# Kernel optimization log

Hardware: AMD Instinct MI355X
Metric: run time of the kernel (lower is better)

Reference implementation:

```python
import jax, jax.numpy as jnp
import numpy as np

HIDDEN = 1024

def setup_inputs() -> dict:
    key = jax.random.key(0)
    k1, k2, k3, k4, k5 = jax.random.split(key, 5)
    B, T, E2, H = 32, 2048, 1024, HIDDEN
    scale = 1.0 / np.sqrt(H)
    x = jax.random.normal(k1, (B, T, E2), dtype=jnp.float32)
    W_ih = jax.random.uniform(k2, (4 * H, E2), minval=-scale, maxval=scale, dtype=jnp.float32)
    W_hh = jax.random.uniform(k3, (4 * H, H), minval=-scale, maxval=scale, dtype=jnp.float32)
    b_ih = jax.random.uniform(k4, (4 * H,), minval=-scale, maxval=scale, dtype=jnp.float32)
    b_hh = jax.random.uniform(k5, (4 * H,), minval=-scale, maxval=scale, dtype=jnp.float32)
    return {"x": x, "W_ih": W_ih, "W_hh": W_hh, "b_ih": b_ih, "b_hh": b_hh}

def reference(x, W_ih, W_hh, b_ih, b_hh):
    B, T, _ = x.shape
    H = W_hh.shape[1]
    # Precompute input contribution for all timesteps: [T, B, 4H]
    x_proj = jnp.einsum('bte,ge->tbg', x, W_ih) + b_ih + b_hh

    def step(carry, xp_t):
        h, c = carry
        gates = xp_t + h @ W_hh.T  # [B, 4H]
        i, f, g, o = jnp.split(gates, 4, axis=-1)  # torch gate order i,f,g,o
        i = jax.nn.sigmoid(i)
        f = jax.nn.sigmoid(f)
        g = jnp.tanh(g)
        o = jax.nn.sigmoid(o)
        c_new = f * c + i * g
        h_new = o * jnp.tanh(c_new)
        return (h_new, c_new), None

    h0 = jnp.zeros((B, H), dtype=x.dtype)
    c0 = jnp.zeros((B, H), dtype=x.dtype)
    (h_t, c_t), _ = jax.lax.scan(step, (h0, c0), x_proj)
    return (h_t, c_t)
```

## Files before the change

### kernel.cpp

```cpp
#include <hip/hip_runtime.h>
#include <stdint.h>

#define T_STEPS 2048
#define HID 1024
#define G4 4096
#define NWG 64

typedef __attribute__((ext_vector_type(8))) short short8;
typedef __attribute__((ext_vector_type(4))) float float4v;
typedef __attribute__((ext_vector_type(4))) unsigned int uint4v;
typedef unsigned long long ull;

#define HBUF_OFF 0ull
#define FLAG_OFF 131072ull
#define DT_OFF   132608ull
#define CST_OFF  135168ull
#define XP_OFF   0x100000ull

__device__ inline unsigned short f2bf(float f) {
  union { float f; unsigned int u; } v; v.f = f;
  unsigned int u = v.u;
  return (unsigned short)((u + 0x7fffu + ((u >> 16) & 1u)) >> 16);
}
__device__ inline float bf2f(unsigned short h) {
  union { unsigned int u; float f; } v; v.u = ((unsigned int)h) << 16;
  return v.f;
}
__device__ inline short8 pack8(float4 a, float4 b) {
  short8 r;
  r[0] = (short)f2bf(a.x); r[1] = (short)f2bf(a.y);
  r[2] = (short)f2bf(a.z); r[3] = (short)f2bf(a.w);
  r[4] = (short)f2bf(b.x); r[5] = (short)f2bf(b.y);
  r[6] = (short)f2bf(b.z); r[7] = (short)f2bf(b.w);
  return r;
}

__global__ void dtype_sniff(const unsigned short* __restrict__ w,
                            unsigned int* __restrict__ dt) {
  __shared__ int red[256];
  const int tid = threadIdx.x;
  int cnt = 0;
#pragma unroll
  for (int i = 0; i < 4; i++) {
    unsigned short h = w[tid * 4 + i];
    unsigned e = (h >> 7) & 0xFF;
    if (h == 0 || (e >= 100 && e <= 123)) cnt++;
  }
  red[tid] = cnt;
  __syncthreads();
  for (int s = 128; s > 0; s >>= 1) {
    if (tid < s) red[tid] += red[tid + s];
    __syncthreads();
  }
  if (tid == 0) dt[0] = (red[0] >= 922) ? 1u : 0u;
}

__global__ __launch_bounds__(256) void xproj_gemm(
    const void* __restrict__ x, const void* __restrict__ Wih,
    const void* __restrict__ bih, const void* __restrict__ bhh,
    unsigned short* __restrict__ xp, int t0,
    const unsigned int* __restrict__ dt)
{
  __shared__ char smem[32768];
  __shared__ float bias_s[128];
  unsigned short* As = (unsigned short*)smem;
  unsigned short* Bs = (unsigned short*)(smem + 10240);

  const bool isbf = (*dt != 0);

  const int bid = blockIdx.x;
  const int panel = bid >> 9;
  const int within = bid & 511;
  const int nt = within & 31;
  const int mt = (panel << 4) + (within >> 5);
  const int m0 = mt * 128;
  const int n0 = nt * 128;
  const int tl0 = m0 >> 5;

  const int tid = threadIdx.x;
  if (tid < 128) {
    bias_s[tid] = isbf
        ? bf2f(((const unsigned short*)bih)[n0 + tid]) +
          bf2f(((const unsigned short*)bhh)[n0 + tid])
        : ((const float*)bih)[n0 + tid] + ((const float*)bhh)[n0 + tid];
  }

  const int w = tid >> 6, lane = tid & 63;
  const int quad = lane >> 4, lr = lane & 15;
  const int wm = (w & 1) * 64, wn = (w >> 1) * 64;

  float4v acc[4][4];
#pragma unroll
  for (int i = 0; i < 4; i++)
#pragma unroll
    for (int j = 0; j < 4; j++) acc[i][j] = (float4v){0.f, 0.f, 0.f, 0.f};

  const int r = tid >> 1, half = tid & 1;
  const size_t aoff =
      ((size_t)(r & 31) * T_STEPS + (size_t)(t0 + tl0 + (r >> 5))) * HID + half * 16;
  const size_t boff = (size_t)(n0 + r) * HID + half * 16;
  unsigned short* adst = As + r * 40 + half * 16;
  unsigned short* bdst = Bs + r * 40 + half * 16;

  for (int k0 = 0; k0 < HID; k0 += 32) {
    __syncthreads();
    if (isbf) {
      const unsigned short* a16 = (const unsigned short*)x + aoff + k0;
      const unsigned short* b16 = (const unsigned short*)Wih + boff + k0;
      *(short8*)(adst)     = *(const short8*)(a16);
      *(short8*)(adst + 8) = *(const short8*)(a16 + 8);
      *(short8*)(bdst)     = *(const short8*)(b16);
      *(short8*)(bdst + 8) = *(const short8*)(b16 + 8);
    } else {
      const float4* af = (const float4*)((const float*)x + aoff + k0);
      const float4* bf = (const float4*)((const float*)Wih + boff + k0);
      float4 a0 = af[0], a1 = af[1], a2 = af[2], a3 = af[3];
      float4 b0 = bf[0], b1 = bf[1], b2 = bf[2], b3 = bf[3];
      *(short8*)(adst)     = pack8(a0, a1);
      *(short8*)(adst + 8) = pack8(a2, a3);
      *(short8*)(bdst)     = pack8(b0, b1);
      *(short8*)(bdst + 8) = pack8(b2, b3);
    }
    __syncthreads();
    short8 afr[4], bfr[4];
#pragma unroll
    for (int i = 0; i < 4; i++)
      afr[i] = *(const short8*)(As + (wm + i * 16 + lr) * 40 + quad * 8);
#pragma unroll
    for (int j = 0; j < 4; j++)
      bfr[j] = *(const short8*)(Bs + (wn + j * 16 + lr) * 40 + quad * 8);
#pragma unroll
    for (int i = 0; i < 4; i++)
#pragma unroll
      for (int j = 0; j < 4; j++)
        acc[i][j] = __builtin_amdgcn_mfma_f32_16x16x32_bf16(afr[i], bfr[j], acc[i][j], 0, 0, 0);
  }

  __syncthreads();
  unsigned short* ep = (unsigned short*)smem;
#pragma unroll
  for (int i = 0; i < 4; i++)
#pragma unroll
    for (int j = 0; j < 4; j++)
#pragma unroll
      for (int rr = 0; rr < 4; rr++) {
        int ml = wm + i * 16 + quad * 4 + rr;
        int nl = wn + j * 16 + lr;
        float v = acc[i][j][rr] + bias_s[nl];
        ep[(((ml >> 5) * 128) + nl) * 32 + (ml & 31)] = f2bf(v);
      }
  __syncthreads();
#pragma unroll
  for (int tl = 0; tl < 4; tl++) {
    const uint4* s4 = (const uint4*)(smem + tl * 8192);
    uint4* d4 = (uint4*)(xp + ((size_t)(tl0 + tl) * G4 + n0) * 32);
    for (int i = tid; i < 512; i += 256) d4[i] = s4[i];
  }
}

__global__ __launch_bounds__(256, 1) void lstm_rec(
    const void* __restrict__ Whh,
    const unsigned short* __restrict__ xp,
    unsigned short* __restrict__ hbuf,
    unsigned int* __restrict__ flags,
    float* __restrict__ cstate,
    void* __restrict__ out,
    int t0, int tc,
    const unsigned int* __restrict__ dt)
{
  __shared__ __align__(16) unsigned short hs[32768];
  __shared__ float gbuf[64][33];

  const bool isbf = (*dt != 0);
  const int wg = blockIdx.x;
  const int tid = threadIdx.x;
  const int w = tid >> 6, lane = tid & 63;
  const int quad = lane >> 4, lr = lane & 15;

  short8 bfrag[32];
  {
    const size_t grow = (size_t)w * HID + wg * 16 + lr;
    if (isbf) {
      const unsigned short* wrow = (const unsigned short*)Whh + grow * HID;
#pragma unroll
      for (int s = 0; s < 32; s++)
        bfrag[s] = *(const short8*)(wrow + s * 32 + quad * 8);
    } else {
      const float* wrow = (const float*)Whh + grow * HID;
#pragma unroll
      for (int s = 0; s < 32; s++) {
        float4 f0 = *(const float4*)(wrow + s * 32 + quad * 8);
        float4 f1 = *(const float4*)(wrow + s * 32 + quad * 8 + 4);
        bfrag[s] = pack8(f0, f1);
      }
    }
  }

  const int gb = lane >> 1, gh = lane & 1;
  const int gc = 2 * w + gh;
  const int gslot = (gc & 3) ^ ((gb >> 1) & 3);
  char* gdst = (char*)hs + ((gc >> 2) * 2048 + gb * 64 + gslot * 16);

  const int qsw = quad ^ ((lr >> 1) & 3);
  const char* ga0 = (const char*)hs + lr * 64 + qsw * 16;
  const char* ga1 = (const char*)hs + (16 + lr) * 64 + qsw * 16;

  const int cb = 8 * w + (lane >> 3);
  const int ck = lane & 7;
  const int j0 = 2 * ck, j1 = j0 + 1;
  const int gc0 = wg * 16 + j0, gc1 = gc0 + 1;
  float cs0 = cstate[(size_t)cb * HID + gc0];
  float cs1 = cstate[(size_t)cb * HID + gc1];
  long budget = 50000000;

  for (int t = t0; t < t0 + tc; t++) {
    const unsigned short* xpt = xp + (size_t)(t - t0) * (G4 * 32);
    unsigned short rx0 = xpt[(size_t)gc0 * 32 + cb];
    unsigned short rx1 = xpt[(size_t)(HID + gc0) * 32 + cb];
    unsigned short rx2 = xpt[(size_t)(2 * HID + gc0) * 32 + cb];
    unsigned short rx3 = xpt[(size_t)(3 * HID + gc0) * 32 + cb];
    unsigned short rx4 = xpt[(size_t)gc1 * 32 + cb];
    unsigned short rx5 = xpt[(size_t)(HID + gc1) * 32 + cb];
    unsigned short rx6 = xpt[(size_t)(2 * HID + gc1) * 32 + cb];
    unsigned short rx7 = xpt[(size_t)(3 * HID + gc1) * 32 + cb];

    if (w == 0) {
      const unsigned target = (unsigned)t;
      const unsigned int* fp = flags + 4 * lane;
      for (;;) {
        uint4v f;
        asm volatile("global_load_dwordx4 %0, %1, off sc0 sc1\n\t"
                     "s_waitcnt vmcnt(0)"
                     : "=v"(f) : "v"(fp) : "memory");
        unsigned m01 = f[0] < f[1] ? f[0] : f[1];
        unsigned m23 = f[2] < f[3] ? f[2] : f[3];
        if ((m01 < m23 ? m01 : m23) >= target) break;
        if (--budget < 0) break;
        __builtin_amdgcn_s_sleep(1);
      }
    }
    __syncthreads();

    {
      const uint4v* src = (const uint4v*)(hbuf + (size_t)(t & 1) * 32768) + tid;
      uint4v v0, v1, v2, v3, v4, v5, v6, v7, v8, v9, v10, v11, v12, v13, v14, v15;
#define GL(i, dst) \
      asm volatile("global_load_dwordx4 %0, %1, off sc0 sc1" \
                   : "=v"(dst) : "v"(src + (i) * 256) : "memory")
      GL(0, v0);  GL(1, v1);  GL(2, v2);  GL(3, v3);
      GL(4, v4);  GL(5, v5);  GL(6, v6);  GL(7, v7);
      GL(8, v8);  GL(9, v9);  GL(10, v10); GL(11, v11);
      GL(12, v12); GL(13, v13); GL(14, v14); GL(15, v15);
#undef GL
      asm volatile("s_waitcnt vmcnt(0)" ::: "memory");
      *(uint4v*)(gdst + 0 * 4096)  = v0;  *(uint4v*)(gdst + 1 * 4096)  = v1;
      *(uint4v*)(gdst + 2 * 4096)  = v2;  *(uint4v*)(gdst + 3 * 4096)  = v3;
      *(uint4v*)(gdst + 4 * 4096)  = v4;  *(uint4v*)(gdst + 5 * 4096)  = v5;
      *(uint4v*)(gdst + 6 * 4096)  = v6;  *(uint4v*)(gdst + 7 * 4096)  = v7;
      *(uint4v*)(gdst + 8 * 4096)  = v8;  *(uint4v*)(gdst + 9 * 4096)  = v9;
      *(uint4v*)(gdst + 10 * 4096) = v10; *(uint4v*)(gdst + 11 * 4096) = v11;
      *(uint4v*)(gdst + 12 * 4096) = v12; *(uint4v*)(gdst + 13 * 4096) = v13;
      *(uint4v*)(gdst + 14 * 4096) = v14; *(uint4v*)(gdst + 15 * 4096) = v15;
    }
    __syncthreads();

    float4v acc00 = (float4v){0.f, 0.f, 0.f, 0.f};
    float4v acc01 = (float4v){0.f, 0.f, 0.f, 0.f};
    float4v acc10 = (float4v){0.f, 0.f, 0.f, 0.f};
    float4v acc11 = (float4v){0.f, 0.f, 0.f, 0.f};
#pragma unroll
    for (int s = 0; s < 32; s += 2) {
      short8 x00 = *(const short8*)(ga0 + (size_t)s * 2048);
      short8 x01 = *(const short8*)(ga0 + (size_t)s * 2048 + 2048);
      short8 x10 = *(const short8*)(ga1 + (size_t)s * 2048);
      short8 x11 = *(const short8*)(ga1 + (size_t)s * 2048 + 2048);
      acc00 = __builtin_amdgcn_mfma_f32_16x16x32_bf16(x00, bfrag[s],     acc00, 0, 0, 0);
      acc01 = __builtin_amdgcn_mfma_f32_16x16x32_bf16(x01, bfrag[s + 1], acc01, 0, 0, 0);
      acc10 = __builtin_amdgcn_mfma_f32_16x16x32_bf16(x10, bfrag[s],     acc10, 0, 0, 0);
      acc11 = __builtin_amdgcn_mfma_f32_16x16x32_bf16(x11, bfrag[s + 1], acc11, 0, 0, 0);
    }
    {
      float4v g0 = acc00 + acc01;
      float4v g1 = acc10 + acc11;
      const int lc = w * 16 + lr;
#pragma unroll
      for (int rr = 0; rr < 4; rr++) {
        gbuf[lc][quad * 4 + rr]      = g0[rr];
        gbuf[lc][16 + quad * 4 + rr] = g1[rr];
      }
    }
    __syncthreads();

    {
      float gi0 = gbuf[j0][cb]      + bf2f(rx0);
      float gf0 = gbuf[16 + j0][cb] + bf2f(rx1);
      float gg0 = gbuf[32 + j0][cb] + bf2f(rx2);
      float go0 = gbuf[48 + j0][cb] + bf2f(rx3);
      float si0 = 1.f / (1.f + __expf(-gi0));
      float sf0 = 1.f / (1.f + __expf(-gf0));
      float tg0 = tanhf(gg0);
      float so0 = 1.f / (1.f + __expf(-go0));
      cs0 = sf0 * cs0 + si0 * tg0;
      float hn0 = so0 * tanhf(cs0);

      float gi1 = gbuf[j1][cb]      + bf2f(rx4);
      float gf1 = gbuf[16 + j1][cb] + bf2f(rx5);
      float gg1 = gbuf[32 + j1][cb] + bf2f(rx6);
      float go1 = gbuf[48 + j1][cb] + bf2f(rx7);
      float si1 = 1.f / (1.f + __expf(-gi1));
      float sf1 = 1.f / (1.f + __expf(-gf1));
      float tg1 = tanhf(gg1);
      float so1 = 1.f / (1.f + __expf(-go1));
      cs1 = sf1 * cs1 + si1 * tg1;
      float hn1 = so1 * tanhf(cs1);

      unsigned pk = (unsigned)f2bf(hn0) | ((unsigned)f2bf(hn1) << 16);
      unsigned int* hb32 = (unsigned int*)hbuf;
      const unsigned idx = (unsigned)(((t + 1) & 1) * 16384 +
                                      wg * 256 + cb * 8 + ck);
      __hip_atomic_store(hb32 + idx, pk, __ATOMIC_RELAXED, __HIP_MEMORY_SCOPE_AGENT);

      if (t == T_STEPS - 1) {
        if (isbf) {
          unsigned short* ob = (unsigned short*)out;
          ob[(size_t)cb * HID + gc0] = f2bf(hn0);
          ob[(size_t)cb * HID + gc1] = f2bf(hn1);
          ob[32768 + (size_t)cb * HID + gc0] = f2bf(cs0);
          ob[32768 + (size_t)cb * HID + gc1] = f2bf(cs1);
        } else {
          float* of = (float*)out;
          of[(size_t)cb * HID + gc0] = hn0;
          of[(size_t)cb * HID + gc1] = hn1;
          of[32768 + (size_t)cb * HID + gc0] = cs0;
          of[32768 + (size_t)cb * HID + gc1] = cs1;
        }
      }
    }
    asm volatile("s_waitcnt vmcnt(0)" ::: "memory");
    if (lane == 0)
      __hip_atomic_store(&flags[wg * 4 + w], (unsigned)(t + 1), __ATOMIC_RELAXED,
                         __HIP_MEMORY_SCOPE_AGENT);
  }

  cstate[(size_t)cb * HID + gc0] = cs0;
  cstate[(size_t)cb * HID + gc1] = cs1;
}

extern "C" void kernel_launch(void* const* d_in, const int* in_sizes, int n_in,
                              void* d_out, int out_size, void* d_ws, size_t ws_size,
                              hipStream_t stream) {
  (void)in_sizes; (void)n_in; (void)out_size;
  const void* x   = d_in[0];
  const void* Wih = d_in[1];
  const void* Whh = d_in[2];
  const void* bih = d_in[3];
  const void* bhh = d_in[4];

  char* ws = (char*)d_ws;
  unsigned short* hbuf   = (unsigned short*)(ws + HBUF_OFF);
  unsigned int*   flags  = (unsigned int*)(ws + FLAG_OFF);
  unsigned int*   dt     = (unsigned int*)(ws + DT_OFF);
  float*          cstate = (float*)(ws + CST_OFF);
  unsigned short* xp     = (unsigned short*)(ws + XP_OFF);

  int tc = 2048;
  while (tc > 16 && XP_OFF + (size_t)tc * 262144ull > ws_size) tc >>= 1;

  hipMemsetAsync(ws, 0, CST_OFF + 131072, stream);

  hipLaunchKernelGGL(dtype_sniff, dim3(1), dim3(256), 0, stream,
                     (const unsigned short*)Wih, dt);

  for (int t0 = 0; t0 < T_STEPS; t0 += tc) {
    hipLaunchKernelGGL(xproj_gemm, dim3(tc * 8), dim3(256), 0, stream,
                       x, Wih, bih, bhh, xp, t0, dt);
    hipLaunchKernelGGL(lstm_rec, dim3(NWG), dim3(256), 0, stream,
                       Whh, xp, hbuf, flags, cstate, d_out, t0, tc, dt);
  }
}
```

Baseline: 12.78 ms.

## Split K across waves and load h directly into MFMA registers

Each wave now owns a quarter of the K dimension for all four gates instead of all K for one gate. Each wave loads its h slice straight from global memory into MFMA operand registers, which removes the shared-memory staging of h and one barrier. Partial sums from the four waves are reduced through a shared buffer. Every wave now polls its own subset of flags instead of only wave 0, which trades a block barrier for more polling traffic. The risk is that the per-wave global loads give less coalesced h fetches.

Result: faster. 11.12 ms (-13.0%).

```diff
diff --git a/kernel.cpp b/kernel.cpp
--- a/kernel.cpp
+++ b/kernel.cpp
@@ -168,8 +168,7 @@
     int t0, int tc,
     const unsigned int* __restrict__ dt)
 {
-  __shared__ __align__(16) unsigned short hs[32768];
-  __shared__ float gbuf[64][33];
+  __shared__ float gpart[4][64][36];
 
   const bool isbf = (*dt != 0);
   const int wg = blockIdx.x;
@@ -178,32 +177,24 @@
   const int quad = lane >> 4, lr = lane & 15;
 
   short8 bfrag[32];
-  {
-    const size_t grow = (size_t)w * HID + wg * 16 + lr;
+#pragma unroll
+  for (int q = 0; q < 4; q++) {
+    const size_t grow = (size_t)q * HID + wg * 16 + lr;
     if (isbf) {
       const unsigned short* wrow = (const unsigned short*)Whh + grow * HID;
 #pragma unroll
-      for (int s = 0; s < 32; s++)
-        bfrag[s] = *(const short8*)(wrow + s * 32 + quad * 8);
+      for (int s = 0; s < 8; s++)
+        bfrag[q * 8 + s] = *(const short8*)(wrow + w * 256 + s * 32 + quad * 8);
     } else {
       const float* wrow = (const float*)Whh + grow * HID;
 #pragma unroll
-      for (int s = 0; s < 32; s++) {
-        float4 f0 = *(const float4*)(wrow + s * 32 + quad * 8);
-        float4 f1 = *(const float4*)(wrow + s * 32 + quad * 8 + 4);
-        bfrag[s] = pack8(f0, f1);
-      }
-    }
-  }
-
-  const int gb = lane >> 1, gh = lane & 1;
-  const int gc = 2 * w + gh;
-  const int gslot = (gc & 3) ^ ((gb >> 1) & 3);
-  char* gdst = (char*)hs + ((gc >> 2) * 2048 + gb * 64 + gslot * 16);
-
-  const int qsw = quad ^ ((lr >> 1) & 3);
-  const char* ga0 = (const char*)hs + lr * 64 + qsw * 16;
-  const char* ga1 = (const char*)hs + (16 + lr) * 64 + qsw * 16;
+      for (int s = 0; s < 8; s++) {
+        float4 f0 = *(const float4*)(wrow + w * 256 + s * 32 + quad * 8);
+        float4 f1 = *(const float4*)(wrow + w * 256 + s * 32 + quad * 8 + 4);
+        bfrag[q * 8 + s] = pack8(f0, f1);
+      }
+    }
+  }
 
   const int cb = 8 * w + (lane >> 3);
   const int ck = lane & 7;
@@ -212,6 +203,8 @@
   float cs0 = cstate[(size_t)cb * HID + gc0];
   float cs1 = cstate[(size_t)cb * HID + gc1];
   long budget = 50000000;
+
+  const int gbase_off = w * 16384 + (quad >> 1) * 1024 + lr * 32 + (quad & 1) * 16;
 
   for (int t = t0; t < t0 + tc; t++) {
     const unsigned short* xpt = xp + (size_t)(t - t0) * (G4 * 32);
@@ -224,78 +217,66 @@
     unsigned short rx6 = xpt[(size_t)(2 * HID + gc1) * 32 + cb];
     unsigned short rx7 = xpt[(size_t)(3 * HID + gc1) * 32 + cb];
 
-    if (w == 0) {
+    {
       const unsigned target = (unsigned)t;
-      const unsigned int* fp = flags + 4 * lane;
-      for (;;) {
-        uint4v f;
-        asm volatile("global_load_dwordx4 %0, %1, off sc0 sc1\n\t"
-                     "s_waitcnt vmcnt(0)"
-                     : "=v"(f) : "v"(fp) : "memory");
-        unsigned m01 = f[0] < f[1] ? f[0] : f[1];
-        unsigned m23 = f[2] < f[3] ? f[2] : f[3];
-        if ((m01 < m23 ? m01 : m23) >= target) break;
+      const unsigned int* fp = flags + 64 * w + lane;
+      while (__hip_atomic_load(fp, __ATOMIC_RELAXED, __HIP_MEMORY_SCOPE_AGENT) < target) {
         if (--budget < 0) break;
         __builtin_amdgcn_s_sleep(1);
       }
     }
-    __syncthreads();
-
+
+    short8 av[2][8];
     {
-      const uint4v* src = (const uint4v*)(hbuf + (size_t)(t & 1) * 32768) + tid;
-      uint4v v0, v1, v2, v3, v4, v5, v6, v7, v8, v9, v10, v11, v12, v13, v14, v15;
-#define GL(i, dst) \
+      const char* gb = (const char*)hbuf + (size_t)(t & 1) * 65536 + gbase_off;
+#define GL(m, s) \
       asm volatile("global_load_dwordx4 %0, %1, off sc0 sc1" \
-                   : "=v"(dst) : "v"(src + (i) * 256) : "memory")
-      GL(0, v0);  GL(1, v1);  GL(2, v2);  GL(3, v3);
-      GL(4, v4);  GL(5, v5);  GL(6, v6);  GL(7, v7);
-      GL(8, v8);  GL(9, v9);  GL(10, v10); GL(11, v11);
-      GL(12, v12); GL(13, v13); GL(14, v14); GL(15, v15);
+                   : "=v"(av[m][s]) : "v"(gb + (s) * 2048 + (m) * 512) : "memory")
+      GL(0, 0); GL(1, 0); GL(0, 1); GL(1, 1);
+      GL(0, 2); GL(1, 2); GL(0, 3); GL(1, 3);
+      GL(0, 4); GL(1, 4); GL(0, 5); GL(1, 5);
+      GL(0, 6); GL(1, 6); GL(0, 7); GL(1, 7);
 #undef GL
       asm volatile("s_waitcnt vmcnt(0)" ::: "memory");
-      *(uint4v*)(gdst + 0 * 4096)  = v0;  *(uint4v*)(gdst + 1 * 4096)  = v1;
-      *(uint4v*)(gdst + 2 * 4096)  = v2;  *(uint4v*)(gdst + 3 * 4096)  = v3;
-      *(uint4v*)(gdst + 4 * 4096)  = v4;  *(uint4v*)(gdst + 5 * 4096)  = v5;
-      *(uint4v*)(gdst + 6 * 4096)  = v6;  *(uint4v*)(gdst + 7 * 4096)  = v7;
-      *(uint4v*)(gdst + 8 * 4096)  = v8;  *(uint4v*)(gdst + 9 * 4096)  = v9;
-      *(uint4v*)(gdst + 10 * 4096) = v10; *(uint4v*)(gdst + 11 * 4096) = v11;
-      *(uint4v*)(gdst + 12 * 4096) = v12; *(uint4v*)(gdst + 13 * 4096) = v13;
-      *(uint4v*)(gdst + 14 * 4096) = v14; *(uint4v*)(gdst + 15 * 4096) = v15;
-    }
-    __syncthreads();
-
-    float4v acc00 = (float4v){0.f, 0.f, 0.f, 0.f};
-    float4v acc01 = (float4v){0.f, 0.f, 0.f, 0.f};
-    float4v acc10 = (float4v){0.f, 0.f, 0.f, 0.f};
-    float4v acc11 = (float4v){0.f, 0.f, 0.f, 0.f};
-#pragma unroll
-    for (int s = 0; s < 32; s += 2) {
-      short8 x00 = *(const short8*)(ga0 + (size_t)s * 2048);
-      short8 x01 = *(const short8*)(ga0 + (size_t)s * 2048 + 2048);
-      short8 x10 = *(const short8*)(ga1 + (size_t)s * 2048);
-      short8 x11 = *(const short8*)(ga1 + (size_t)s * 2048 + 2048);
-      acc00 = __builtin_amdgcn_mfma_f32_16x16x32_bf16(x00, bfrag[s],     acc00, 0, 0, 0);
-      acc01 = __builtin_amdgcn_mfma_f32_16x16x32_bf16(x01, bfrag[s + 1], acc01, 0, 0, 0);
-      acc10 = __builtin_amdgcn_mfma_f32_16x16x32_bf16(x10, bfrag[s],     acc10, 0, 0, 0);
-      acc11 = __builtin_amdgcn_mfma_f32_16x16x32_bf16(x11, bfrag[s + 1], acc11, 0, 0, 0);
-    }
+      __builtin_amdgcn_sched_barrier(0);
+    }
+
+    float4v acc[2][4];
+#pragma unroll
+    for (int m = 0; m < 2; m++)
+#pragma unroll
+      for (int q = 0; q < 4; q++) acc[m][q] = (float4v){0.f, 0.f, 0.f, 0.f};
+#pragma unroll
+    for (int s = 0; s < 8; s++) {
+#pragma unroll
+      for (int q = 0; q < 4; q++) {
+        acc[0][q] = __builtin_amdgcn_mfma_f32_16x16x32_bf16(av[0][s], bfrag[q * 8 + s], acc[0][q], 0, 0, 0);
+        acc[1][q] = __builtin_amdgcn_mfma_f32_16x16x32_bf16(av[1][s], bfrag[q * 8 + s], acc[1][q], 0, 0, 0);
+      }
+    }
+
+    __syncthreads();
+#pragma unroll
+    for (int m = 0; m < 2; m++)
+#pragma unroll
+      for (int q = 0; q < 4; q++)
+        *(float4v*)&gpart[w][q * 16 + lr][m * 16 + quad * 4] = acc[m][q];
+    __syncthreads();
+
     {
-      float4v g0 = acc00 + acc01;
-      float4v g1 = acc10 + acc11;
-      const int lc = w * 16 + lr;
-#pragma unroll
-      for (int rr = 0; rr < 4; rr++) {
-        gbuf[lc][quad * 4 + rr]      = g0[rr];
-        gbuf[lc][16 + quad * 4 + rr] = g1[rr];
-      }
-    }
-    __syncthreads();
-
-    {
-      float gi0 = gbuf[j0][cb]      + bf2f(rx0);
-      float gf0 = gbuf[16 + j0][cb] + bf2f(rx1);
-      float gg0 = gbuf[32 + j0][cb] + bf2f(rx2);
-      float go0 = gbuf[48 + j0][cb] + bf2f(rx3);
+      float gi0 = bf2f(rx0), gf0 = bf2f(rx1), gg0 = bf2f(rx2), go0 = bf2f(rx3);
+      float gi1 = bf2f(rx4), gf1 = bf2f(rx5), gg1 = bf2f(rx6), go1 = bf2f(rx7);
+#pragma unroll
+      for (int p = 0; p < 4; p++) {
+        gi0 += gpart[p][j0][cb];
+        gf0 += gpart[p][16 + j0][cb];
+        gg0 += gpart[p][32 + j0][cb];
+        go0 += gpart[p][48 + j0][cb];
+        gi1 += gpart[p][j1][cb];
+        gf1 += gpart[p][16 + j1][cb];
+        gg1 += gpart[p][32 + j1][cb];
+        go1 += gpart[p][48 + j1][cb];
+      }
       float si0 = 1.f / (1.f + __expf(-gi0));
       float sf0 = 1.f / (1.f + __expf(-gf0));
       float tg0 = tanhf(gg0);
@@ -303,10 +284,6 @@
       cs0 = sf0 * cs0 + si0 * tg0;
       float hn0 = so0 * tanhf(cs0);
 
-      float gi1 = gbuf[j1][cb]      + bf2f(rx4);
-      float gf1 = gbuf[16 + j1][cb] + bf2f(rx5);
-      float gg1 = gbuf[32 + j1][cb] + bf2f(rx6);
-      float go1 = gbuf[48 + j1][cb] + bf2f(rx7);
       float si1 = 1.f / (1.f + __expf(-gi1));
       float sf1 = 1.f / (1.f + __expf(-gf1));
       float tg1 = tanhf(gg1);
@@ -316,8 +293,7 @@
 
       unsigned pk = (unsigned)f2bf(hn0) | ((unsigned)f2bf(hn1) << 16);
       unsigned int* hb32 = (unsigned int*)hbuf;
-      const unsigned idx = (unsigned)(((t + 1) & 1) * 16384 +
-                                      wg * 256 + cb * 8 + ck);
+      const unsigned idx = (unsigned)(((t + 1) & 1) * 16384 + wg * 256 + cb * 8 + ck);
       __hip_atomic_store(hb32 + idx, pk, __ATOMIC_RELAXED, __HIP_MEMORY_SCOPE_AGENT);
 
       if (t == T_STEPS - 1) {
```
